# Performance work log

Measured on AMD Instinct MI355X. Metric: run time of the kernel, lower is better.

Reference implementation:

```python
import jax, jax.numpy as jnp
import numpy as np

B, N, C, H = 2, 2048, 1024, 16
D = C // H  # head_dim = 64


def setup_inputs() -> dict:
    key = jax.random.key(0)
    kx, kq, kk, kv, ko = jax.random.split(key, 5)
    # xavier_uniform bound for square (C, C) matrices
    bound = float(np.sqrt(6.0 / (C + C)))
    u = lambda k: jax.random.uniform(k, (C, C), jnp.float32, -bound, bound)
    return {
        "x": jax.random.normal(kx, (B, N, C), jnp.float32),
        "W_q": u(kq),
        "W_k": u(kk),
        "W_v": u(kv),
        "W_o": u(ko),
    }


def reference(x, W_q, W_k, W_v, W_o):
    # quantum_linear == dense matmul (no bias); tomography_error_delta=0 -> identity
    b, n, c = x.shape
    q = jnp.einsum("bnc,cd->bnd", x, W_q).reshape(b, n, H, D).transpose(0, 2, 1, 3)
    k = jnp.einsum("bnc,cd->bnd", x, W_k).reshape(b, n, H, D).transpose(0, 2, 1, 3)
    v = jnp.einsum("bnc,cd->bnd", x, W_v).reshape(b, n, H, D).transpose(0, 2, 1, 3)
    # scaled dot-product attention, [B, H, N, N]
    scores = jnp.einsum("bhnd,bhmd->bhnm", q, k) / jnp.sqrt(jnp.float32(D))
    weights = jax.nn.softmax(scores, axis=-1)
    heads = jnp.einsum("bhnm,bhmd->bhnd", weights, v)  # [B, H, N, D]
    concat = heads.transpose(0, 2, 1, 3).reshape(b, n, c)
    out = jnp.einsum("bnc,cd->bnd", concat, W_o)
    return out
```

## Files before the change

kernel.cpp:

```cpp
#include <hip/hip_runtime.h>

typedef __attribute__((ext_vector_type(4))) float f32x4;
typedef __attribute__((ext_vector_type(8))) short s16x8;
typedef unsigned int u32;
typedef __attribute__((ext_vector_type(4))) unsigned int u32x4;

#define B_ 2
#define N_ 2048
#define C_ 1024
#define H_ 16
#define D_ 64

__device__ __forceinline__ unsigned short f2bf(float f) {
  union { float f; unsigned u; } v; v.f = f;
  unsigned r = v.u + 0x7fffu + ((v.u >> 16) & 1u);
  return (unsigned short)(r >> 16);
}

__global__ __launch_bounds__(256) void wtrans_kernel(
    const float* __restrict__ Wq, const float* __restrict__ Wk,
    const float* __restrict__ Wv, const float* __restrict__ Wo,
    unsigned short* __restrict__ WtQKV, unsigned short* __restrict__ WtO,
    const float* __restrict__ xsrc, unsigned short* __restrict__ xb) {
  const int t = threadIdx.x;
  if (blockIdx.x >= 1024) {
    int i = (blockIdx.x - 1024) * 2048 + t * 8;
    float4 f0 = *(const float4*)&xsrc[i];
    float4 f1 = *(const float4*)&xsrc[i + 4];
    u32 p0, p1, p2, p3;
    asm("v_cvt_pk_bf16_f32 %0, %1, %2" : "=v"(p0) : "v"(f0.x), "v"(f0.y));
    asm("v_cvt_pk_bf16_f32 %0, %1, %2" : "=v"(p1) : "v"(f0.z), "v"(f0.w));
    asm("v_cvt_pk_bf16_f32 %0, %1, %2" : "=v"(p2) : "v"(f1.x), "v"(f1.y));
    asm("v_cvt_pk_bf16_f32 %0, %1, %2" : "=v"(p3) : "v"(f1.z), "v"(f1.w));
    uint4 o; o.x = p0; o.y = p1; o.z = p2; o.w = p3;
    *(uint4*)&xb[i] = o;
    return;
  }
  __shared__ float lds[64][65];
  const int w = blockIdx.x >> 8;
  const int tile = blockIdx.x & 255;
  const int c0 = (tile >> 4) * 64, d0 = (tile & 15) * 64;
  const float* W = (w == 0) ? Wq : (w == 1) ? Wk : (w == 2) ? Wv : Wo;
  const float scale = (w == 0) ? 0.125f * 1.4426950408889634f : 1.0f;
  #pragma unroll
  for (int p = 0; p < 16; ++p) {
    int i = p * 256 + t; int r = i >> 6, cc = i & 63;
    lds[r][cc] = W[(size_t)(c0 + r) * 1024 + d0 + cc];
  }
  __syncthreads();
  #pragma unroll
  for (int p = 0; p < 16; ++p) {
    int i = p * 256 + t; int r = i >> 6, cc = i & 63;
    unsigned short v = f2bf(lds[cc][r] * scale);
    if (w < 3) WtQKV[(size_t)(w * 1024 + d0 + r) * 1024 + c0 + cc] = v;
    else       WtO[(size_t)(d0 + r) * 1024 + c0 + cc] = v;
  }
}

template <int MODE>
__global__ __launch_bounds__(256, 3) void gemm_kernel(
    const unsigned short* __restrict__ A, const unsigned short* __restrict__ Bt,
    unsigned short* __restrict__ Qh, unsigned short* __restrict__ Kh,
    unsigned short* __restrict__ Vt, float* __restrict__ Cf) {
  __shared__ __align__(16) unsigned short GS[24576];
  unsigned short* Asb = GS;
  unsigned short* Bsb = GS + 12288;
  const int tid = threadIdx.x;
  const int lane = tid & 63, wv = tid >> 6;
  const int g = lane >> 4, c = lane & 15;
  const int wr = wv >> 1, wc = wv & 1;
  const int am0 = blockIdx.x * 128;
  const int bn0 = blockIdx.y * 128;

  f32x4 acc[4][4];
  #pragma unroll
  for (int m = 0; m < 4; m++)
    #pragma unroll
    for (int n = 0; n < 4; n++) acc[m][n] = (f32x4){0.f, 0.f, 0.f, 0.f};

  const int srow = (lane >> 2);
  const int schunk = (lane & 3) ^ (srow & 3);

#define GSTAGE(buf, k0s)                                                       \
  do {                                                                         \
    _Pragma("unroll")                                                          \
    for (int i = 0; i < 2; ++i) {                                              \
      int row = i * 64 + wv * 16 + srow;                                       \
      __builtin_amdgcn_global_load_lds(                                        \
          (const __attribute__((address_space(1))) void*)(                     \
              A + (size_t)(am0 + row) * 1024 + (k0s) + schunk * 8),            \
          (__attribute__((address_space(3))) void*)(Asb + (buf)*4096 +         \
              (i * 64 + wv * 16) * 32),                                        \
          16, 0, 0);                                                           \
      __builtin_amdgcn_global_load_lds(                                        \
          (const __attribute__((address_space(1))) void*)(                     \
              Bt + (size_t)(bn0 + row) * 1024 + (k0s) + schunk * 8),           \
          (__attribute__((address_space(3))) void*)(Bsb + (buf)*4096 +         \
              (i * 64 + wv * 16) * 32),                                        \
          16, 0, 0);                                                           \
    }                                                                          \
  } while (0)

  GSTAGE(0, 0);
  GSTAGE(1, 32);
  asm volatile("s_waitcnt vmcnt(4)" ::: "memory");
  __builtin_amdgcn_s_barrier();
  __builtin_amdgcn_sched_barrier(0);

  for (int kt = 0; kt < 32; ++kt) {
    const int cur = kt % 3;
    s16x8 af[4], bfr[4];
    #pragma unroll
    for (int m = 0; m < 4; m++) {
      int R = wr * 64 + m * 16 + c;
      af[m] = *(const s16x8*)&Asb[cur * 4096 + R * 32 + ((g ^ (R & 3)) << 3)];
    }
    #pragma unroll
    for (int n = 0; n < 4; n++) {
      int R = wc * 64 + n * 16 + c;
      bfr[n] = *(const s16x8*)&Bsb[cur * 4096 + R * 32 + ((g ^ (R & 3)) << 3)];
    }
    if (kt < 30) GSTAGE((kt + 2) % 3, (kt + 2) * 32);
    __builtin_amdgcn_s_setprio(1);
    #pragma unroll
    for (int m = 0; m < 4; m++)
      #pragma unroll
      for (int n = 0; n < 4; n++)
        acc[m][n] = __builtin_amdgcn_mfma_f32_16x16x32_bf16(af[m], bfr[n], acc[m][n], 0, 0, 0);
    __builtin_amdgcn_s_setprio(0);
    __builtin_amdgcn_sched_barrier(0);
    asm volatile("s_waitcnt lgkmcnt(0)" ::: "memory");
    if (kt < 30) {
      asm volatile("s_waitcnt vmcnt(4)" ::: "memory");
    } else if (kt == 30) {
      asm volatile("s_waitcnt vmcnt(0)" ::: "memory");
    }
    __builtin_amdgcn_sched_barrier(0);
    __builtin_amdgcn_s_barrier();
    __builtin_amdgcn_sched_barrier(0);
  }
#undef GSTAGE

  const bool vblock = (MODE == 0) && (blockIdx.y >= 16);
  if (!vblock) {
    #pragma unroll
    for (int m = 0; m < 4; m++) {
      #pragma unroll
      for (int n = 0; n < 4; n++) {
        f32x4 v = acc[m][n];
        int colg = bn0 + wc * 64 + n * 16 + c;
        #pragma unroll
        for (int r = 0; r < 4; ++r) {
          int row = am0 + wr * 64 + m * 16 + g * 4 + r;
          if (MODE == 1) {
            Cf[(size_t)row * 1024 + colg] = v[r];
          } else {
            int tensor = colg >> 10, cc = colg & 1023;
            int hh = cc >> 6, dd = cc & 63;
            int bb = row >> 11, tok = row & 2047;
            unsigned short val = f2bf(v[r]);
            if (tensor == 0)
              Qh[(((size_t)bb * H_ + hh) * N_ + tok) * D_ + dd] = val;
            else
              Kh[(((size_t)bb * H_ + hh) * N_ + tok) * D_ + dd] = val;
          }
        }
      }
    }
  } else {
    __syncthreads();
    #pragma unroll
    for (int m = 0; m < 4; m++) {
      #pragma unroll
      for (int n = 0; n < 4; n++) {
        f32x4 v = acc[m][n];
        int lc = wc * 64 + n * 16 + c;
        #pragma unroll
        for (int r = 0; r < 4; ++r) {
          int lr = wr * 64 + m * 16 + g * 4 + r;
          GS[lc * 128 + ((((lr >> 3) ^ (lc & 15)) << 3) | (lr & 7))] = f2bf(v[r]);
        }
      }
    }
    __syncthreads();
    const int chl = tid & 15, rowb = tid >> 4;
    const int tok0 = (am0 & 2047) + chl * 8;
    const int bb = am0 >> 11;
    #pragma unroll
    for (int j = 0; j < 8; ++j) {
      int ddl = j * 16 + rowb;
      s16x8 val = *(const s16x8*)&GS[ddl * 128 + ((chl ^ (ddl & 15)) << 3)];
      int vcol = bn0 - 2048 + ddl;
      int hh = vcol >> 6, dd = vcol & 63;
      *(s16x8*)&Vt[(((size_t)bb * H_ + hh) * D_ + dd) * N_ + tok0] = val;
    }
  }
}

__global__ __launch_bounds__(512, 2) void attn_kernel(
    const unsigned short* __restrict__ Qh, const unsigned short* __restrict__ Kh,
    const unsigned short* __restrict__ Vt, unsigned short* __restrict__ heads) {
  __shared__ unsigned short Ks[2][128 * 64];
  __shared__ unsigned short Vs[3][64 * 128];
  const int tid = threadIdx.x;
  const int lane = tid & 63, wv = tid >> 6;
  const int g = lane >> 4, c = lane & 15;
  const int c7 = c & 7;
  const int xcd = blockIdx.x & 7, idx = blockIdx.x >> 3;
  const int bh = xcd * 4 + (idx >> 3), qb = idx & 7;
  const int b = bh >> 4, h = bh & 15;
  const int q0 = qb * 256 + wv * 32;

  const unsigned short* Qbase = Qh + ((size_t)bh * N_ + q0) * D_;
  const unsigned short* Kbase = Kh + (size_t)bh * N_ * D_;
  const unsigned short* Vbase = Vt + (size_t)bh * D_ * N_;

  s16x8 qfrag[2][2];
  #pragma unroll
  for (int qf = 0; qf < 2; ++qf)
    #pragma unroll
    for (int dblk = 0; dblk < 2; ++dblk)
      qfrag[qf][dblk] =
          *(const s16x8*)&Qbase[(size_t)(qf * 16 + c) * D_ + dblk * 32 + g * 8];

  s16x8 ones;
  #pragma unroll
  for (int j = 0; j < 8; ++j) ones[j] = (short)0x3F80;

  f32x4 O[2][4];
  f32x4 L[2];
  #pragma unroll
  for (int qf = 0; qf < 2; ++qf) {
    #pragma unroll
    for (int db = 0; db < 4; ++db) O[qf][db] = (f32x4){0.f, 0.f, 0.f, 0.f};
    L[qf] = (f32x4){0.f, 0.f, 0.f, 0.f};
  }

#define STAGE(kbuf, vbuf, t)                                                   \
  do {                                                                         \
    const int kv0s = (t) * 128;                                                \
    _Pragma("unroll")                                                          \
    for (int i = 0; i < 2; ++i) {                                              \
      int row = i * 64 + wv * 8 + (lane >> 3);                                 \
      int un = (lane & 7) ^ (row & 7);                                         \
      __builtin_amdgcn_global_load_lds(                                        \
          (const __attribute__((address_space(1))) void*)(Kbase +              \
              (size_t)(kv0s + row) * 64 + un * 8),                             \
          (__attribute__((address_space(3))) void*)(&Ks[kbuf][(i * 512 + wv * 64) * 8]), \
          16, 0, 0);                                                           \
    }                                                                          \
    _Pragma("unroll")                                                          \
    for (int i = 0; i < 2; ++i) {                                              \
      int vrow = i * 32 + wv * 4 + (lane >> 4);                                \
      int un = (lane & 15) ^ (vrow & 15);                                      \
      __builtin_amdgcn_global_load_lds(                                        \
          (const __attribute__((address_space(1))) void*)(Vbase +              \
              (size_t)vrow * N_ + kv0s + un * 8),                              \
          (__attribute__((address_space(3))) void*)(&Vs[vbuf][(i * 512 + wv * 64) * 8]), \
          16, 0, 0);                                                           \
    }                                                                          \
  } while (0)

#define PVSTEP(VBUF, PF)                                                       \
  do {                                                                         \
    _Pragma("unroll")                                                          \
    for (int km = 0; km < 4; ++km) {                                           \
      union { u32x4 u; s16x8 s; } b0_, b1_;                                    \
      b0_.u = (u32x4){PF[0][km][0], PF[0][km][1], PF[0][km][2], PF[0][km][3]}; \
      b1_.u = (u32x4){PF[1][km][0], PF[1][km][1], PF[1][km][2], PF[1][km][3]}; \
      _Pragma("unroll")                                                        \
      for (int db = 0; db < 4; ++db) {                                         \
        s16x8 vf = *(const s16x8*)&Vs[VBUF][(db * 16 + c) * 128 +              \
                                           (((km * 4 + g) ^ c) << 3)];         \
        O[0][db] = __builtin_amdgcn_mfma_f32_16x16x32_bf16(vf, b0_.s, O[0][db], 0, 0, 0); \
        O[1][db] = __builtin_amdgcn_mfma_f32_16x16x32_bf16(vf, b1_.s, O[1][db], 0, 0, 0); \
      }                                                                        \
      L[0] = __builtin_amdgcn_mfma_f32_16x16x32_bf16(ones, b0_.s, L[0], 0, 0, 0); \
      L[1] = __builtin_amdgcn_mfma_f32_16x16x32_bf16(ones, b1_.s, L[1], 0, 0, 0); \
    }                                                                          \
  } while (0)

  u32 pf[2][4][4], pfp[2][4][4];

  STAGE(0, 0, 0);
  __syncthreads();

  #pragma unroll
  for (int t = 0; t < 16; ++t) {
    const int kcur = t & 1;
    if (t < 15) STAGE((t + 1) & 1, (t + 1) % 3, t + 1);

    f32x4 st[2][8];
    __builtin_amdgcn_s_setprio(1);
    #pragma unroll
    for (int kb = 0; kb < 8; ++kb) {
      s16x8 k0 = *(const s16x8*)&Ks[kcur][(kb * 16 + c) * 64 + ((g ^ c7) << 3)];
      s16x8 k1 = *(const s16x8*)&Ks[kcur][(kb * 16 + c) * 64 + (((4 + g) ^ c7) << 3)];
      #pragma unroll
      for (int qf = 0; qf < 2; ++qf) {
        f32x4 z = (f32x4){0.f, 0.f, 0.f, 0.f};
        z = __builtin_amdgcn_mfma_f32_16x16x32_bf16(k0, qfrag[qf][0], z, 0, 0, 0);
        st[qf][kb] = __builtin_amdgcn_mfma_f32_16x16x32_bf16(k1, qfrag[qf][1], z, 0, 0, 0);
      }
    }
    __builtin_amdgcn_s_setprio(0);

    if (t > 0) {
      PVSTEP((t + 2) % 3, pfp);
    }

    #pragma unroll
    for (int qf = 0; qf < 2; ++qf) {
      #pragma unroll
      for (int kb = 0; kb < 8; ++kb)
        #pragma unroll
        for (int r = 0; r < 4; ++r)
          st[qf][kb][r] = __builtin_amdgcn_exp2f(st[qf][kb][r]);

      #pragma unroll
      for (int km = 0; km < 4; ++km) {
        u32 x00, x01, x10, x11;
        asm("v_cvt_pk_bf16_f32 %0, %1, %2" : "=v"(x00) : "v"(st[qf][2 * km][0]), "v"(st[qf][2 * km][1]));
        asm("v_cvt_pk_bf16_f32 %0, %1, %2" : "=v"(x01) : "v"(st[qf][2 * km][2]), "v"(st[qf][2 * km][3]));
        asm("v_cvt_pk_bf16_f32 %0, %1, %2" : "=v"(x10) : "v"(st[qf][2 * km + 1][0]), "v"(st[qf][2 * km + 1][1]));
        asm("v_cvt_pk_bf16_f32 %0, %1, %2" : "=v"(x11) : "v"(st[qf][2 * km + 1][2]), "v"(st[qf][2 * km + 1][3]));
        asm("v_permlane32_swap_b32 %0, %1" : "+v"(x00), "+v"(x10));
        asm("v_permlane32_swap_b32 %0, %1" : "+v"(x01), "+v"(x11));
        asm("v_permlane16_swap_b32 %0, %1" : "+v"(x00), "+v"(x10));
        asm("v_permlane16_swap_b32 %0, %1" : "+v"(x01), "+v"(x11));
        pf[qf][km][0] = x00; pf[qf][km][1] = x01;
        pf[qf][km][2] = x10; pf[qf][km][3] = x11;
      }
    }

    #pragma unroll
    for (int qf = 0; qf < 2; ++qf)
      #pragma unroll
      for (int km = 0; km < 4; ++km)
        #pragma unroll
        for (int j = 0; j < 4; ++j) pfp[qf][km][j] = pf[qf][km][j];

    __syncthreads();
  }

  __builtin_amdgcn_s_setprio(1);
  PVSTEP(0, pfp);
  __builtin_amdgcn_s_setprio(0);
#undef STAGE
#undef PVSTEP

  #pragma unroll
  for (int qf = 0; qf < 2; ++qf) {
    float linv = 1.0f / L[qf][0];
    size_t rowoff = ((size_t)(b * N_ + q0 + qf * 16 + c)) * C_ + h * 64;
    #pragma unroll
    for (int db = 0; db < 4; ++db) {
      u32 d0, d1;
      float v0 = O[qf][db][0] * linv, v1 = O[qf][db][1] * linv;
      float v2 = O[qf][db][2] * linv, v3 = O[qf][db][3] * linv;
      asm("v_cvt_pk_bf16_f32 %0, %1, %2" : "=v"(d0) : "v"(v0), "v"(v1));
      asm("v_cvt_pk_bf16_f32 %0, %1, %2" : "=v"(d1) : "v"(v2), "v"(v3));
      uint2 st2; st2.x = d0; st2.y = d1;
      *(uint2*)&heads[rowoff + db * 16 + g * 4] = st2;
    }
  }
}

extern "C" void kernel_launch(void* const* d_in, const int* in_sizes, int n_in,
                              void* d_out, int out_size, void* d_ws, size_t ws_size,
                              hipStream_t stream) {
  const float* x  = (const float*)d_in[0];
  const float* Wq = (const float*)d_in[1];
  const float* Wk = (const float*)d_in[2];
  const float* Wv = (const float*)d_in[3];
  const float* Wo = (const float*)d_in[4];
  float* out = (float*)d_out;

  char* ws = (char*)d_ws;
  unsigned short* WtQKV = (unsigned short*)(ws);
  unsigned short* WtO   = (unsigned short*)(ws + 6291456);
  unsigned short* Qh    = (unsigned short*)(ws + 8388608);
  unsigned short* Kh    = (unsigned short*)(ws + 16777216);
  unsigned short* Vt    = (unsigned short*)(ws + 25165824);
  unsigned short* heads = (unsigned short*)(ws + 33554432);
  unsigned short* xb    = (unsigned short*)(ws + 33554432);

  wtrans_kernel<<<dim3(3072), dim3(256), 0, stream>>>(Wq, Wk, Wv, Wo, WtQKV, WtO, x, xb);
  gemm_kernel<0><<<dim3(32, 24), dim3(256), 0, stream>>>(xb, WtQKV, Qh, Kh, Vt, nullptr);
  attn_kernel<<<dim3(256), dim3(512), 0, stream>>>(Qh, Kh, Vt, heads);
  gemm_kernel<1><<<dim3(32, 8), dim3(256), 0, stream>>>(heads, WtO, nullptr, nullptr, nullptr, out);
}
```

Measured before the change: 99.37 us.

## Use 256x256-tile 8-wave ping-pong GEMM for the QKV projection

Replaces the templated 128x128 GEMM for the fused QKV projection with a dedicated 512-thread kernel using 256x256 tiles, 128 KB of LDS double buffering, and a fine-grained schedule that interleaves LDS fragment loads, global-to-LDS staging and MFMA quarter-blocks between barriers. The grid drops from 768 to 192 blocks, raising arithmetic intensity per LDS byte and reducing global traffic for the 4096x3072x1024 GEMM. The output GEMM keeps the old kernel, now specialised without the mode template. Risks are fewer blocks than a full wave across the 256 CUs, heavy register pressure from 32 accumulators, and many barriers per iteration.

Result: faster. 96.51 us, median of 2 (-2.9%).

```diff
diff --git a/kernel.cpp b/kernel.cpp
--- a/kernel.cpp
+++ b/kernel.cpp
@@ -57,11 +57,193 @@
   }
 }
 
-template <int MODE>
-__global__ __launch_bounds__(256, 3) void gemm_kernel(
+__global__ __launch_bounds__(512, 2) void gemm0_kernel(
     const unsigned short* __restrict__ A, const unsigned short* __restrict__ Bt,
     unsigned short* __restrict__ Qh, unsigned short* __restrict__ Kh,
-    unsigned short* __restrict__ Vt, float* __restrict__ Cf) {
+    unsigned short* __restrict__ Vt) {
+  __shared__ __align__(16) unsigned short GS[65536];
+  const int tid = threadIdx.x;
+  const int lane = tid & 63, wv = tid >> 6;
+  const int g = lane >> 4, c = lane & 15;
+  const int c7 = c & 7;
+  const int wr = wv >> 2, wc = wv & 3;
+  const int am0 = blockIdx.x * 256;
+  const int bn0 = blockIdx.y * 256;
+  const int srow8 = lane >> 3;
+  const int schunk = (lane & 7) ^ (srow8 & 7);
+
+  enum { A0o = 0, A1o = 16384, B0o = 32768, B1o = 49152 };
+
+  f32x4 acc[8][4];
+  #pragma unroll
+  for (int m = 0; m < 8; ++m)
+    #pragma unroll
+    for (int n = 0; n < 4; ++n) acc[m][n] = (f32x4){0.f, 0.f, 0.f, 0.f};
+
+  s16x8 af[4][2];
+  s16x8 bfr[4][2];
+
+#define STAGE(P, rb, ldsOff, h, kslab)                                         \
+  do {                                                                         \
+    _Pragma("unroll")                                                          \
+    for (int i_ = 0; i_ < 2; ++i_) {                                           \
+      __builtin_amdgcn_global_load_lds(                                        \
+          (const __attribute__((address_space(1))) void*)(                     \
+              (P) + (size_t)((rb) + (h) * 128 + i_ * 64 + wv * 8 + srow8) *    \
+                        1024 + (kslab) * 64 + schunk * 8),                     \
+          (__attribute__((address_space(3))) void*)(GS + (ldsOff) +            \
+              ((h) * 128 + i_ * 64 + wv * 8) * 64),                            \
+          16, 0, 0);                                                           \
+    }                                                                          \
+  } while (0)
+
+#define LDA(bufOff, mh)                                                        \
+  do {                                                                         \
+    _Pragma("unroll")                                                          \
+    for (int mm = 0; mm < 4; ++mm)                                             \
+      _Pragma("unroll")                                                        \
+      for (int kk = 0; kk < 2; ++kk)                                           \
+        af[mm][kk] = *(const s16x8*)&GS[(bufOff) +                             \
+            (((mh) * 4 + mm) * 32 + wr * 16 + c) * 64 +                        \
+            (((kk * 4 + g) ^ c7) << 3)];                                       \
+  } while (0)
+
+#define LDB(bufOff, nh)                                                        \
+  do {                                                                         \
+    _Pragma("unroll")                                                          \
+    for (int nn = 0; nn < 2; ++nn)                                             \
+      _Pragma("unroll")                                                        \
+      for (int kk = 0; kk < 2; ++kk)                                           \
+        bfr[(nh) * 2 + nn][kk] = *(const s16x8*)&GS[(bufOff) +                 \
+            ((((nh) * 2 + nn) * 64 + wc * 16 + c)) * 64 +                      \
+            (((kk * 4 + g) ^ c7) << 3)];                                       \
+  } while (0)
+
+#define MM(mh, nh)                                                             \
+  do {                                                                         \
+    __builtin_amdgcn_s_setprio(1);                                             \
+    _Pragma("unroll")                                                          \
+    for (int mm = 0; mm < 4; ++mm)                                             \
+      _Pragma("unroll")                                                        \
+      for (int nn = 0; nn < 2; ++nn)                                           \
+        _Pragma("unroll")                                                      \
+        for (int kk = 0; kk < 2; ++kk)                                         \
+          acc[(mh) * 4 + mm][(nh) * 2 + nn] =                                  \
+              __builtin_amdgcn_mfma_f32_16x16x32_bf16(                         \
+                  af[mm][kk], bfr[(nh) * 2 + nn][kk],                          \
+                  acc[(mh) * 4 + mm][(nh) * 2 + nn], 0, 0, 0);                 \
+    __builtin_amdgcn_s_setprio(0);                                             \
+  } while (0)
+
+#define BAR() __builtin_amdgcn_s_barrier()
+#define LGKM0() asm volatile("s_waitcnt lgkmcnt(0)" ::: "memory")
+
+  STAGE(A, am0, A0o, 0, 0);
+  STAGE(Bt, bn0, B0o, 0, 0);
+  STAGE(A, am0, A0o, 1, 0);
+  STAGE(Bt, bn0, B0o, 1, 0);
+  STAGE(A, am0, A1o, 0, 1);
+  STAGE(Bt, bn0, B1o, 0, 1);
+  STAGE(A, am0, A1o, 1, 1);
+  asm volatile("s_waitcnt vmcnt(6)" ::: "memory");
+  BAR();
+
+  for (int it = 0; it < 8; ++it) {
+    const int kc = 2 * it + 2, kd = 2 * it + 3;
+    const bool more = (it < 7);
+    LDA(A0o, 0); LDB(B0o, 0);
+    STAGE(Bt, bn0, B1o, 1, 2 * it + 1);
+    BAR(); LGKM0(); MM(0, 0); BAR();
+    LDB(B0o, 1);
+    if (more) STAGE(A, am0, A0o, 0, kc);
+    BAR(); LGKM0(); MM(0, 1); BAR();
+    LDA(A0o, 1);
+    if (more) STAGE(Bt, bn0, B0o, 0, kc);
+    BAR(); LGKM0(); MM(1, 0); BAR();
+    if (more) {
+      STAGE(A, am0, A0o, 1, kc);
+      asm volatile("s_waitcnt vmcnt(6)" ::: "memory");
+    } else {
+      asm volatile("s_waitcnt vmcnt(0)" ::: "memory");
+    }
+    BAR(); LGKM0(); MM(1, 1); BAR();
+    LDA(A1o, 0); LDB(B1o, 0);
+    if (more) STAGE(Bt, bn0, B0o, 1, kc);
+    BAR(); LGKM0(); MM(0, 0); BAR();
+    LDB(B1o, 1);
+    if (more) STAGE(A, am0, A1o, 0, kd);
+    BAR(); LGKM0(); MM(0, 1); BAR();
+    LDA(A1o, 1);
+    if (more) STAGE(Bt, bn0, B1o, 0, kd);
+    BAR(); LGKM0(); MM(1, 0); BAR();
+    if (more) {
+      STAGE(A, am0, A1o, 1, kd);
+      asm volatile("s_waitcnt vmcnt(6)" ::: "memory");
+    }
+    BAR(); LGKM0(); MM(1, 1); BAR();
+  }
+#undef STAGE
+#undef LDA
+#undef LDB
+#undef MM
+#undef BAR
+#undef LGKM0
+
+  const bool vblock = (blockIdx.y >= 8);
+  if (!vblock) {
+    #pragma unroll
+    for (int m = 0; m < 8; ++m) {
+      #pragma unroll
+      for (int n = 0; n < 4; ++n) {
+        f32x4 v = acc[m][n];
+        int colg = bn0 + n * 64 + wc * 16 + c;
+        int tensor = colg >> 10, cc = colg & 1023;
+        int hh = cc >> 6, dd = cc & 63;
+        #pragma unroll
+        for (int r = 0; r < 4; ++r) {
+          int row = am0 + m * 32 + wr * 16 + g * 4 + r;
+          int bb = row >> 11, tok = row & 2047;
+          unsigned short val = f2bf(v[r]);
+          if (tensor == 0)
+            Qh[(((size_t)bb * H_ + hh) * N_ + tok) * D_ + dd] = val;
+          else
+            Kh[(((size_t)bb * H_ + hh) * N_ + tok) * D_ + dd] = val;
+        }
+      }
+    }
+  } else {
+    __syncthreads();
+    #pragma unroll
+    for (int m = 0; m < 8; ++m) {
+      #pragma unroll
+      for (int n = 0; n < 4; ++n) {
+        f32x4 v = acc[m][n];
+        int lc = n * 64 + wc * 16 + c;
+        #pragma unroll
+        for (int r = 0; r < 4; ++r) {
+          int lr = m * 32 + wr * 16 + g * 4 + r;
+          GS[lc * 256 + ((((lr >> 3) ^ (lc & 31)) << 3) | (lr & 7))] = f2bf(v[r]);
+        }
+      }
+    }
+    __syncthreads();
+    const int chl = tid & 31, rowb = tid >> 5;
+    const int tok0 = (am0 & 2047) + chl * 8;
+    const int bb = am0 >> 11;
+    #pragma unroll
+    for (int j = 0; j < 16; ++j) {
+      int ddl = j * 16 + rowb;
+      s16x8 val = *(const s16x8*)&GS[ddl * 256 + ((chl ^ (ddl & 31)) << 3)];
+      int vcol = bn0 - 2048 + ddl;
+      int hh = vcol >> 6, dd = vcol & 63;
+      *(s16x8*)&Vt[(((size_t)bb * H_ + hh) * D_ + dd) * N_ + tok0] = val;
+    }
+  }
+}
+
+__global__ __launch_bounds__(256, 3) void gemm1_kernel(
+    const unsigned short* __restrict__ A, const unsigned short* __restrict__ Bt,
+    float* __restrict__ Cf) {
   __shared__ __align__(16) unsigned short GS[24576];
   unsigned short* Asb = GS;
   unsigned short* Bsb = GS + 12288;
@@ -141,58 +323,17 @@
   }
 #undef GSTAGE
 
-  const bool vblock = (MODE == 0) && (blockIdx.y >= 16);
-  if (!vblock) {
-    #pragma unroll
-    for (int m = 0; m < 4; m++) {
-      #pragma unroll
-      for (int n = 0; n < 4; n++) {
-        f32x4 v = acc[m][n];
-        int colg = bn0 + wc * 64 + n * 16 + c;
-        #pragma unroll
-        for (int r = 0; r < 4; ++r) {
-          int row = am0 + wr * 64 + m * 16 + g * 4 + r;
-          if (MODE == 1) {
-            Cf[(size_t)row * 1024 + colg] = v[r];
-          } else {
-            int tensor = colg >> 10, cc = colg & 1023;
-            int hh = cc >> 6, dd = cc & 63;
-            int bb = row >> 11, tok = row & 2047;
-            unsigned short val = f2bf(v[r]);
-            if (tensor == 0)
-              Qh[(((size_t)bb * H_ + hh) * N_ + tok) * D_ + dd] = val;
-            else
-              Kh[(((size_t)bb * H_ + hh) * N_ + tok) * D_ + dd] = val;
-          }
-        }
+  #pragma unroll
+  for (int m = 0; m < 4; m++) {
+    #pragma unroll
+    for (int n = 0; n < 4; n++) {
+      f32x4 v = acc[m][n];
+      int colg = bn0 + wc * 64 + n * 16 + c;
+      #pragma unroll
+      for (int r = 0; r < 4; ++r) {
+        int row = am0 + wr * 64 + m * 16 + g * 4 + r;
+        Cf[(size_t)row * 1024 + colg] = v[r];
       }
-    }
-  } else {
-    __syncthreads();
-    #pragma unroll
-    for (int m = 0; m < 4; m++) {
-      #pragma unroll
-      for (int n = 0; n < 4; n++) {
-        f32x4 v = acc[m][n];
-        int lc = wc * 64 + n * 16 + c;
-        #pragma unroll
-        for (int r = 0; r < 4; ++r) {
-          int lr = wr * 64 + m * 16 + g * 4 + r;
-          GS[lc * 128 + ((((lr >> 3) ^ (lc & 15)) << 3) | (lr & 7))] = f2bf(v[r]);
-        }
-      }
-    }
-    __syncthreads();
-    const int chl = tid & 15, rowb = tid >> 4;
-    const int tok0 = (am0 & 2047) + chl * 8;
-    const int bb = am0 >> 11;
-    #pragma unroll
-    for (int j = 0; j < 8; ++j) {
-      int ddl = j * 16 + rowb;
-      s16x8 val = *(const s16x8*)&GS[ddl * 128 + ((chl ^ (ddl & 15)) << 3)];
-      int vcol = bn0 - 2048 + ddl;
-      int hh = vcol >> 6, dd = vcol & 63;
-      *(s16x8*)&Vt[(((size_t)bb * H_ + hh) * D_ + dd) * N_ + tok0] = val;
     }
   }
 }
@@ -386,7 +527,7 @@
   unsigned short* xb    = (unsigned short*)(ws + 33554432);
 
   wtrans_kernel<<<dim3(3072), dim3(256), 0, stream>>>(Wq, Wk, Wv, Wo, WtQKV, WtO, x, xb);
-  gemm_kernel<0><<<dim3(32, 24), dim3(256), 0, stream>>>(xb, WtQKV, Qh, Kh, Vt, nullptr);
+  gemm0_kernel<<<dim3(16, 12), dim3(512), 0, stream>>>(xb, WtQKV, Qh, Kh, Vt);
   attn_kernel<<<dim3(256), dim3(512), 0, stream>>>(Qh, Kh, Vt, heads);
-  gemm_kernel<1><<<dim3(32, 8), dim3(256), 0, stream>>>(heads, WtO, nullptr, nullptr, nullptr, out);
+  gemm1_kernel<<<dim3(32, 8), dim3(256), 0, stream>>>(heads, WtO, out);
 }
```
